# Optimization experiments

Measured on AMD Instinct MI355X. Metric: run time of the kernel, lower is better.

## Reference

```python
import jax, jax.numpy as jnp
import numpy as np

W = 131072          # window size (number of observed frames)
J = 21              # number of joints
B = J - 1           # number of bones
F, PX, PY = 512.0, 512.0, 288.0   # pinhole intrinsics (SIZE_X=1024, SIZE_Y=576)
EPS = 1e-8
WEIGHTS = {"proj": 0.25, "lift": 0.25, "bone": 0.25, "smooth": 0.25}


def _euler_batch(roll, pitch, yaw):
    """Vectorized ZYX euler -> rotation matrices, numpy, [N,3,3]."""
    cr, sr = np.cos(roll), np.sin(roll)
    cp, sp = np.cos(pitch), np.sin(pitch)
    cy, sy = np.cos(yaw), np.sin(yaw)
    R = np.empty(roll.shape + (3, 3), np.float32)
    R[..., 0, 0] = cy * cp; R[..., 0, 1] = cy * sp * sr - sy * cr; R[..., 0, 2] = cy * sp * cr + sy * sr
    R[..., 1, 0] = sy * cp; R[..., 1, 1] = sy * sp * sr + cy * cr; R[..., 1, 2] = sy * sp * cr - cy * sr
    R[..., 2, 0] = -sp;     R[..., 2, 1] = cp * sr;                R[..., 2, 2] = cp * cr
    return R


def setup_inputs() -> dict:
    key = jax.random.key(0)
    ks = jax.random.split(key, 7)
    pose3d = jax.random.normal(ks[0], (W + 1, 3, J), jnp.float32)
    bone_2d = jax.random.normal(ks[1], (W, 2, J), jnp.float32)
    lift_dirs = jax.random.normal(ks[2], (W, 3, B), jnp.float32)
    # small proper drone rotations so the projection depth stays well away from 0
    ang = 0.05 * np.asarray(jax.random.normal(ks[3], (W, 3)))
    R_drone = jnp.asarray(_euler_batch(ang[:, 0], ang[:, 1], ang[:, 2]))
    # drone positions offset so pose - C_drone ~ +10 in every coordinate
    C_drone = 0.1 * jax.random.normal(ks[4], (W, 3, 1), jnp.float32) - 10.0
    bone_lengths = jax.random.uniform(ks[5], (B,), jnp.float32, 0.5, 1.5)
    R_cam = jnp.asarray(_euler_batch(np.zeros(1), np.full(1, np.pi / 2), np.zeros(1))[0])
    # chain skeleton: bone i connects joint i+1 -> joint i
    bone_connections = jnp.stack([jnp.arange(1, J, dtype=jnp.int32),
                                  jnp.arange(0, J - 1, dtype=jnp.int32)], axis=1)
    return {"pose3d": pose3d, "bone_2d": bone_2d, "lift_dirs": lift_dirs,
            "R_drone": R_drone, "C_drone": C_drone, "bone_lengths": bone_lengths,
            "R_cam": R_cam, "bone_connections": bone_connections}


def _forward(pose3d, bone_2d, lift_dirs, R_drone, C_drone, bone_lengths, R_cam,
             bone_connections):
    Jn = pose3d.shape[2]
    b0 = bone_connections[:, 0]
    b1 = bone_connections[:, 1]
    p = pose3d[1:]                                   # [W,3,J] frames with observations

    # ---- projection loss: cam = R_cam @ R_drone^T @ (p - C_drone), pinhole
    rel = p - C_drone                                # [W,3,J]
    cam = jnp.einsum('ij,wkj,wkn->win', R_cam, R_drone, rel)  # [W,3,J]
    z = cam[:, 2]
    proj2d = jnp.stack([F * cam[:, 0] / z + PX,
                        F * cam[:, 1] / z + PY], axis=1)       # [W,2,J]
    proj_loss = jnp.sum((proj2d - bone_2d) ** 2) / (2 * Jn)

    # ---- lift loss: unit bone direction vectors vs lifted directions
    bv = p[:, :, b0] - p[:, :, b1]                   # [W,3,B]
    dirs = bv / (jnp.linalg.norm(bv, axis=1, keepdims=True) + EPS)
    lift_loss = jnp.sum((lift_dirs - dirs) ** 2) / (3 * Jn)

    # ---- bone-length loss over all W+1 frames (squared lengths, as in torch code)
    bvall = pose3d[:, :, b0] - pose3d[:, :, b1]      # [W+1,3,B]
    blen = jnp.sum(bvall ** 2, axis=1)               # [W+1,B]
    bone_loss = jnp.sum((bone_lengths[None, :] - blen) ** 2) / (Jn - 1)

    # ---- smoothness: second difference of the pose trajectory
    d = pose3d[1:] - pose3d[:-1]                     # [W,3,J]
    smooth_loss = jnp.sum((d[1:] - d[:-1]) ** 2) / (3 * Jn)

    return (WEIGHTS["proj"] * proj_loss + WEIGHTS["lift"] * lift_loss
            + WEIGHTS["bone"] * bone_loss + WEIGHTS["smooth"] * smooth_loss)


def reference(pose3d, bone_2d, lift_dirs, R_drone, C_drone, bone_lengths, R_cam,
              bone_connections):
    return _forward(pose3d, bone_2d, lift_dirs, R_drone, C_drone, bone_lengths,
                    R_cam, bone_connections)
```

## Files before the change

### kernel.cpp

```cpp
#include <hip/hip_runtime.h>

namespace {

constexpr int JN = 21;
constexpr int BN = 20;
constexpr int FR = 64;
constexpr int HT = 32;
constexpr int SPLIT0 = 36;

constexpr float F_F  = 512.0f;
constexpr float PX_F = 512.0f;
constexpr float PY_F = 288.0f;
constexpr float EPS_F = 1e-8f;

constexpr float WPROJ   = 0.25f / (2.0f * 21.0f);
constexpr float WLIFT   = 0.25f / (3.0f * 21.0f);
constexpr float WBONE   = 0.25f / 20.0f;
constexpr float WSMOOTH = 0.25f / (3.0f * 21.0f);

__device__ __forceinline__ double block_reduce(double val) {
    __shared__ double smem[16];
    const int lane = threadIdx.x & 63;
    const int wid  = threadIdx.x >> 6;
    #pragma unroll
    for (int off = 32; off > 0; off >>= 1)
        val += __shfl_down(val, off, 64);
    if (lane == 0) smem[wid] = val;
    __syncthreads();
    if (wid == 0) {
        const int nw = blockDim.x >> 6;
        val = (lane < nw) ? smem[lane] : 0.0;
        #pragma unroll
        for (int off = 32; off > 0; off >>= 1)
            val += __shfl_down(val, off, 64);
    }
    return val;
}

__global__ __launch_bounds__(256) void pose_loss_kernel(
    const float* __restrict__ pose3d,
    const float* __restrict__ bone_2d,
    const float* __restrict__ lift_dirs,
    const float* __restrict__ R_drone,
    const float* __restrict__ C_drone,
    const float* __restrict__ bone_len,
    const float* __restrict__ R_cam,
    float* __restrict__ partials,
    int W)
{
    __shared__ alignas(16) float s_pose[(FR + 2) * 63 + 2];
    __shared__ alignas(16) float s_M[FR * 12];

    const int tid = threadIdx.x;
    const int w0  = blockIdx.x * FR;
    const int nF  = min(FR, W - w0);
    const int nPoseF = min(FR + 2, W + 1 - w0);

    auto stage4 = [&](float* dst, const float* src, int nfl) {
        const int n4 = nfl >> 2;
        const float4* s4 = (const float4*)src;
        float4* d4 = (float4*)dst;
        for (int i = tid; i < n4; i += 256) d4[i] = s4[i];
        for (int i = (n4 << 2) + tid; i < nfl; i += 256) dst[i] = src[i];
    };

    auto computeM = [&](int base) {
        const int f = base + tid;
        if (tid < HT && f < nF) {
            const float* Rd = R_drone + (size_t)(w0 + f) * 9;
            float rd[9];
            #pragma unroll
            for (int k = 0; k < 9; ++k) rd[k] = Rd[k];
            float rc[9];
            #pragma unroll
            for (int k = 0; k < 9; ++k) rc[k] = R_cam[k];
            float M[9];
            #pragma unroll
            for (int i = 0; i < 3; ++i)
                #pragma unroll
                for (int k = 0; k < 3; ++k)
                    M[i * 3 + k] = rc[i * 3 + 0] * rd[k * 3 + 0]
                                 + rc[i * 3 + 1] * rd[k * 3 + 1]
                                 + rc[i * 3 + 2] * rd[k * 3 + 2];
            const float* Cp = C_drone + (size_t)(w0 + f) * 3;
            const float C0 = Cp[0], C1 = Cp[1], C2 = Cp[2];
            #pragma unroll
            for (int k = 0; k < 9; ++k) s_M[f * 12 + k] = M[k];
            #pragma unroll
            for (int i = 0; i < 3; ++i)
                s_M[f * 12 + 9 + i] =
                    M[i * 3 + 0] * C0 + M[i * 3 + 1] * C1 + M[i * 3 + 2] * C2;
        }
    };

    float partial = 0.0f;

    auto item = [&](int wl, int j) {
        const int w = w0 + wl;

        const float* P1 = s_pose + (wl + 1) * 63;
        const float p1x = P1[j];
        const float p1y = P1[JN + j];
        const float p1z = P1[2 * JN + j];

        {
            const float4 m0 = *(const float4*)(s_M + wl * 12);
            const float4 m1 = *(const float4*)(s_M + wl * 12 + 4);
            const float4 m2 = *(const float4*)(s_M + wl * 12 + 8);
            const float c0 = m0.x * p1x + m0.y * p1y + m0.z * p1z - m2.y;
            const float c1 = m0.w * p1x + m1.x * p1y + m1.y * p1z - m2.z;
            const float c2 = m1.z * p1x + m1.w * p1y + m2.x * p1z - m2.w;
            const float invz = 1.0f / c2;
            const float u = F_F * c0 * invz + PX_F;
            const float v = F_F * c1 * invz + PY_F;
            const float du = u - bone_2d[(size_t)w * 42 + j];
            const float dv = v - bone_2d[(size_t)w * 42 + JN + j];
            partial += WPROJ * (du * du + dv * dv);
        }

        if (j < BN) {
            const int b0 = j + 1;
            const int b1 = j;
            {
                const float ax = P1[b0]          - P1[b1];
                const float ay = P1[JN + b0]     - P1[JN + b1];
                const float az = P1[2 * JN + b0] - P1[2 * JN + b1];
                const float inv = 1.0f / (sqrtf(ax * ax + ay * ay + az * az) + EPS_F);
                const float lx = lift_dirs[(size_t)w * 60 + j]          - ax * inv;
                const float ly = lift_dirs[(size_t)w * 60 + BN + j]     - ay * inv;
                const float lz = lift_dirs[(size_t)w * 60 + 2 * BN + j] - az * inv;
                partial += WLIFT * (lx * lx + ly * ly + lz * lz);
            }
            const float blj = bone_len[j];
            {
                const float* P0 = s_pose + wl * 63;
                const float bx = P0[b0]          - P0[b1];
                const float by = P0[JN + b0]     - P0[JN + b1];
                const float bz = P0[2 * JN + b0] - P0[2 * JN + b1];
                const float bl = bx * bx + by * by + bz * bz;
                const float e = blj - bl;
                partial += WBONE * (e * e);
            }
            if (w == W - 1) {
                const float bx = P1[b0]          - P1[b1];
                const float by = P1[JN + b0]     - P1[JN + b1];
                const float bz = P1[2 * JN + b0] - P1[2 * JN + b1];
                const float bl = bx * bx + by * by + bz * bz;
                const float e = blj - bl;
                partial += WBONE * (e * e);
            }
        }

        if (w < W - 1) {
            const float* P0 = s_pose + wl * 63;
            const float* P2 = s_pose + (wl + 2) * 63;
            const float sx = P2[j]          - 2.0f * p1x + P0[j];
            const float sy = P2[JN + j]     - 2.0f * p1y + P0[JN + j];
            const float sz = P2[2 * JN + j] - 2.0f * p1z + P0[2 * JN + j];
            partial += WSMOOTH * (sx * sx + sy * sy + sz * sz);
        }
    };

    {
        const int f1 = min(SPLIT0, nPoseF);
        stage4(s_pose, pose3d + (size_t)w0 * 63, f1 * 63);
        computeM(0);
    }
    __syncthreads();

    if (nPoseF > SPLIT0) {
        stage4(s_pose + SPLIT0 * 63, pose3d + ((size_t)w0 + SPLIT0) * 63,
               (nPoseF - SPLIT0) * 63);
    }
    computeM(HT);

    {
        const int nItems0 = min(HT, nF) * JN;
        for (int it = tid; it < nItems0; it += 256) {
            const int wl = it / JN;
            const int j  = it - wl * JN;
            item(wl, j);
        }
    }
    __syncthreads();

    if (nF > HT) {
        const int nItems1 = (nF - HT) * JN;
        for (int it = tid; it < nItems1; it += 256) {
            const int wl = HT + it / JN;
            const int j  = it - (it / JN) * JN;
            item(wl, j);
        }
    }

    const double bsum = block_reduce((double)partial);
    if (tid == 0) partials[blockIdx.x] = (float)bsum;
}

__global__ __launch_bounds__(256) void final_reduce_kernel(
    const float* __restrict__ partials, float* __restrict__ out, int n)
{
    double v = 0.0;
    for (int i = threadIdx.x; i < n; i += blockDim.x)
        v += (double)partials[i];
    v = block_reduce(v);
    if (threadIdx.x == 0) out[0] = (float)v;
}

}

extern "C" void kernel_launch(void* const* d_in, const int* in_sizes, int n_in,
                              void* d_out, int out_size, void* d_ws, size_t ws_size,
                              hipStream_t stream) {
    const float* pose3d    = (const float*)d_in[0];
    const float* bone_2d   = (const float*)d_in[1];
    const float* lift_dirs = (const float*)d_in[2];
    const float* R_drone   = (const float*)d_in[3];
    const float* C_drone   = (const float*)d_in[4];
    const float* bone_len  = (const float*)d_in[5];
    const float* R_cam     = (const float*)d_in[6];
    float* out = (float*)d_out;
    float* partials = (float*)d_ws;

    const int W = in_sizes[3] / 9;
    const int grid = (W + FR - 1) / FR;

    pose_loss_kernel<<<grid, 256, 0, stream>>>(
        pose3d, bone_2d, lift_dirs, R_drone, C_drone, bone_len, R_cam, partials, W);
    final_reduce_kernel<<<1, 256, 0, stream>>>(partials, out, grid);
}
```

Measured before the change: 27.27 us.

## Split block work into independent per-wavefront frame slices without block barriers

Each 64-lane wavefront now stages its own 16-frame pose slice (plus 2 halo frames) and its own camera matrices into a private shared-memory region, then computes its 21x16 items. This removes the two block-wide __syncthreads and the two-phase split pipeline. It relies on wavefront-level ordering of shared-memory writes and reads. The halo frames add some redundant pose loads per wave, and the full-slice case uses a fixed unrolled item loop.

```diff
diff --git a/kernel.cpp b/kernel.cpp
--- a/kernel.cpp
+++ b/kernel.cpp
@@ -4,9 +4,10 @@
 
 constexpr int JN = 21;
 constexpr int BN = 20;
+constexpr int FW = 16;
 constexpr int FR = 64;
-constexpr int HT = 32;
-constexpr int SPLIT0 = 36;
+constexpr int SLICE = FW + 2;
+constexpr int SLICE_STRIDE = 1136;
 
 constexpr float F_F  = 512.0f;
 constexpr float PX_F = 512.0f;
@@ -48,26 +49,35 @@
     float* __restrict__ partials,
     int W)
 {
-    __shared__ alignas(16) float s_pose[(FR + 2) * 63 + 2];
-    __shared__ alignas(16) float s_M[FR * 12];
-
-    const int tid = threadIdx.x;
+    __shared__ alignas(16) float s_pose[4][SLICE_STRIDE];
+    __shared__ alignas(16) float s_M[4][FW * 12];
+
+    const int tid  = threadIdx.x;
+    const int lane = tid & 63;
+    const int wid  = tid >> 6;
+
     const int w0  = blockIdx.x * FR;
-    const int nF  = min(FR, W - w0);
-    const int nPoseF = min(FR + 2, W + 1 - w0);
-
-    auto stage4 = [&](float* dst, const float* src, int nfl) {
-        const int n4 = nfl >> 2;
-        const float4* s4 = (const float4*)src;
-        float4* d4 = (float4*)dst;
-        for (int i = tid; i < n4; i += 256) d4[i] = s4[i];
-        for (int i = (n4 << 2) + tid; i < nfl; i += 256) dst[i] = src[i];
-    };
-
-    auto computeM = [&](int base) {
-        const int f = base + tid;
-        if (tid < HT && f < nF) {
-            const float* Rd = R_drone + (size_t)(w0 + f) * 9;
+    const int fw0 = w0 + wid * FW;
+    const int nFw = min(FW, W - fw0);
+    float* myPose = s_pose[wid];
+    float* myM    = s_M[wid];
+
+    float partial = 0.0f;
+
+    if (nFw > 0) {
+        {
+            const int nSliceF = min(SLICE, W + 1 - fw0);
+            const int nfl = nSliceF * 63;
+            const float* src = pose3d + (size_t)fw0 * 63;
+            const int n4 = nfl >> 2;
+            const float4* s4 = (const float4*)src;
+            float4* d4 = (float4*)myPose;
+            for (int i = lane; i < n4; i += 64) d4[i] = s4[i];
+            for (int i = (n4 << 2) + lane; i < nfl; i += 64) myPose[i] = src[i];
+        }
+
+        if (lane < FW && lane < nFw) {
+            const float* Rd = R_drone + (size_t)(fw0 + lane) * 9;
             float rd[9];
             #pragma unroll
             for (int k = 0; k < 9; ++k) rd[k] = Rd[k];
@@ -82,114 +92,95 @@
                     M[i * 3 + k] = rc[i * 3 + 0] * rd[k * 3 + 0]
                                  + rc[i * 3 + 1] * rd[k * 3 + 1]
                                  + rc[i * 3 + 2] * rd[k * 3 + 2];
-            const float* Cp = C_drone + (size_t)(w0 + f) * 3;
+            const float* Cp = C_drone + (size_t)(fw0 + lane) * 3;
             const float C0 = Cp[0], C1 = Cp[1], C2 = Cp[2];
             #pragma unroll
-            for (int k = 0; k < 9; ++k) s_M[f * 12 + k] = M[k];
+            for (int k = 0; k < 9; ++k) myM[lane * 12 + k] = M[k];
             #pragma unroll
             for (int i = 0; i < 3; ++i)
-                s_M[f * 12 + 9 + i] =
+                myM[lane * 12 + 9 + i] =
                     M[i * 3 + 0] * C0 + M[i * 3 + 1] * C1 + M[i * 3 + 2] * C2;
         }
-    };
-
-    float partial = 0.0f;
-
-    auto item = [&](int wl, int j) {
-        const int w = w0 + wl;
-
-        const float* P1 = s_pose + (wl + 1) * 63;
-        const float p1x = P1[j];
-        const float p1y = P1[JN + j];
-        const float p1z = P1[2 * JN + j];
-
-        {
-            const float4 m0 = *(const float4*)(s_M + wl * 12);
-            const float4 m1 = *(const float4*)(s_M + wl * 12 + 4);
-            const float4 m2 = *(const float4*)(s_M + wl * 12 + 8);
-            const float c0 = m0.x * p1x + m0.y * p1y + m0.z * p1z - m2.y;
-            const float c1 = m0.w * p1x + m1.x * p1y + m1.y * p1z - m2.z;
-            const float c2 = m1.z * p1x + m1.w * p1y + m2.x * p1z - m2.w;
-            const float invz = 1.0f / c2;
-            const float u = F_F * c0 * invz + PX_F;
-            const float v = F_F * c1 * invz + PY_F;
-            const float du = u - bone_2d[(size_t)w * 42 + j];
-            const float dv = v - bone_2d[(size_t)w * 42 + JN + j];
-            partial += WPROJ * (du * du + dv * dv);
-        }
-
-        if (j < BN) {
-            const int b0 = j + 1;
-            const int b1 = j;
+
+        auto item = [&](int wl, int j) {
+            const int w = fw0 + wl;
+
+            const float* P1 = myPose + (wl + 1) * 63;
+            const float p1x = P1[j];
+            const float p1y = P1[JN + j];
+            const float p1z = P1[2 * JN + j];
+
             {
-                const float ax = P1[b0]          - P1[b1];
-                const float ay = P1[JN + b0]     - P1[JN + b1];
-                const float az = P1[2 * JN + b0] - P1[2 * JN + b1];
-                const float inv = 1.0f / (sqrtf(ax * ax + ay * ay + az * az) + EPS_F);
-                const float lx = lift_dirs[(size_t)w * 60 + j]          - ax * inv;
-                const float ly = lift_dirs[(size_t)w * 60 + BN + j]     - ay * inv;
-                const float lz = lift_dirs[(size_t)w * 60 + 2 * BN + j] - az * inv;
-                partial += WLIFT * (lx * lx + ly * ly + lz * lz);
-            }
-            const float blj = bone_len[j];
-            {
-                const float* P0 = s_pose + wl * 63;
-                const float bx = P0[b0]          - P0[b1];
-                const float by = P0[JN + b0]     - P0[JN + b1];
-                const float bz = P0[2 * JN + b0] - P0[2 * JN + b1];
-                const float bl = bx * bx + by * by + bz * bz;
-                const float e = blj - bl;
-                partial += WBONE * (e * e);
-            }
-            if (w == W - 1) {
-                const float bx = P1[b0]          - P1[b1];
-                const float by = P1[JN + b0]     - P1[JN + b1];
-                const float bz = P1[2 * JN + b0] - P1[2 * JN + b1];
-                const float bl = bx * bx + by * by + bz * bz;
-                const float e = blj - bl;
-                partial += WBONE * (e * e);
-            }
-        }
-
-        if (w < W - 1) {
-            const float* P0 = s_pose + wl * 63;
-            const float* P2 = s_pose + (wl + 2) * 63;
-            const float sx = P2[j]          - 2.0f * p1x + P0[j];
-            const float sy = P2[JN + j]     - 2.0f * p1y + P0[JN + j];
-            const float sz = P2[2 * JN + j] - 2.0f * p1z + P0[2 * JN + j];
-            partial += WSMOOTH * (sx * sx + sy * sy + sz * sz);
-        }
-    };
-
-    {
-        const int f1 = min(SPLIT0, nPoseF);
-        stage4(s_pose, pose3d + (size_t)w0 * 63, f1 * 63);
-        computeM(0);
-    }
-    __syncthreads();
-
-    if (nPoseF > SPLIT0) {
-        stage4(s_pose + SPLIT0 * 63, pose3d + ((size_t)w0 + SPLIT0) * 63,
-               (nPoseF - SPLIT0) * 63);
-    }
-    computeM(HT);
-
-    {
-        const int nItems0 = min(HT, nF) * JN;
-        for (int it = tid; it < nItems0; it += 256) {
-            const int wl = it / JN;
-            const int j  = it - wl * JN;
-            item(wl, j);
-        }
-    }
-    __syncthreads();
-
-    if (nF > HT) {
-        const int nItems1 = (nF - HT) * JN;
-        for (int it = tid; it < nItems1; it += 256) {
-            const int wl = HT + it / JN;
-            const int j  = it - (it / JN) * JN;
-            item(wl, j);
+                const float4 m0 = *(const float4*)(myM + wl * 12);
+                const float4 m1 = *(const float4*)(myM + wl * 12 + 4);
+                const float4 m2 = *(const float4*)(myM + wl * 12 + 8);
+                const float c0 = m0.x * p1x + m0.y * p1y + m0.z * p1z - m2.y;
+                const float c1 = m0.w * p1x + m1.x * p1y + m1.y * p1z - m2.z;
+                const float c2 = m1.z * p1x + m1.w * p1y + m2.x * p1z - m2.w;
+                const float invz = 1.0f / c2;
+                const float u = F_F * c0 * invz + PX_F;
+                const float v = F_F * c1 * invz + PY_F;
+                const float du = u - bone_2d[(size_t)w * 42 + j];
+                const float dv = v - bone_2d[(size_t)w * 42 + JN + j];
+                partial += WPROJ * (du * du + dv * dv);
+            }
+
+            if (j < BN) {
+                const int b0 = j + 1;
+                const int b1 = j;
+                {
+                    const float ax = P1[b0]          - P1[b1];
+                    const float ay = P1[JN + b0]     - P1[JN + b1];
+                    const float az = P1[2 * JN + b0] - P1[2 * JN + b1];
+                    const float inv = 1.0f / (sqrtf(ax * ax + ay * ay + az * az) + EPS_F);
+                    const float lx = lift_dirs[(size_t)w * 60 + j]          - ax * inv;
+                    const float ly = lift_dirs[(size_t)w * 60 + BN + j]     - ay * inv;
+                    const float lz = lift_dirs[(size_t)w * 60 + 2 * BN + j] - az * inv;
+                    partial += WLIFT * (lx * lx + ly * ly + lz * lz);
+                }
+                const float blj = bone_len[j];
+                {
+                    const float* P0 = myPose + wl * 63;
+                    const float bx = P0[b0]          - P0[b1];
+                    const float by = P0[JN + b0]     - P0[JN + b1];
+                    const float bz = P0[2 * JN + b0] - P0[2 * JN + b1];
+                    const float bl = bx * bx + by * by + bz * bz;
+                    const float e = blj - bl;
+                    partial += WBONE * (e * e);
+                }
+                if (w == W - 1) {
+                    const float bx = P1[b0]          - P1[b1];
+                    const float by = P1[JN + b0]     - P1[JN + b1];
+                    const float bz = P1[2 * JN + b0] - P1[2 * JN + b1];
+                    const float bl = bx * bx + by * by + bz * bz;
+                    const float e = blj - bl;
+                    partial += WBONE * (e * e);
+                }
+            }
+
+            if (w < W - 1) {
+                const float* P0 = myPose + wl * 63;
+                const float* P2 = myPose + (wl + 2) * 63;
+                const float sx = P2[j]          - 2.0f * p1x + P0[j];
+                const float sy = P2[JN + j]     - 2.0f * p1y + P0[JN + j];
+                const float sz = P2[2 * JN + j] - 2.0f * p1z + P0[2 * JN + j];
+                partial += WSMOOTH * (sx * sx + sy * sy + sz * sz);
+            }
+        };
+
+        if (nFw == FW) {
+            #pragma unroll
+            for (int k = 0; k < 5; ++k) {
+                const int it = k * 64 + lane;
+                item(it / JN, it - (it / JN) * JN);
+            }
+            if (lane < 16) {
+                const int it = 5 * 64 + lane;
+                item(it / JN, it - (it / JN) * JN);
+            }
+        } else {
+            for (int it = lane; it < nFw * JN; it += 64)
+                item(it / JN, it - (it / JN) * JN);
         }
     }
 
```

Measured after the change: 28.91 us. 1.06x slower.

## Process four joints per thread with vectorized loads and single-stage staging

Applied to the files above, without the earlier changes.

Replaces the per-(frame,joint) work item with chunks of four joints per thread, so neighbouring pose values are loaded once into registers and reused across the projection, lift, bone and smoothness terms. lift_dirs and bone_len are now read as float4. The two-phase staged pipeline (split pose copy and split M computation with overlapped work) becomes one full stage followed by a single barrier. This cuts the shared-memory reads and divisions per element, but 384 chunks over 256 threads leaves the second pass half-occupied and removes the previous load/compute overlap.

```diff
diff --git a/kernel.cpp b/kernel.cpp
--- a/kernel.cpp
+++ b/kernel.cpp
@@ -5,8 +5,6 @@
 constexpr int JN = 21;
 constexpr int BN = 20;
 constexpr int FR = 64;
-constexpr int HT = 32;
-constexpr int SPLIT0 = 36;
 
 constexpr float F_F  = 512.0f;
 constexpr float PX_F = 512.0f;
@@ -56,141 +54,166 @@
     const int nF  = min(FR, W - w0);
     const int nPoseF = min(FR + 2, W + 1 - w0);
 
-    auto stage4 = [&](float* dst, const float* src, int nfl) {
+    {
+        const float* src = pose3d + (size_t)w0 * 63;
+        const int nfl = nPoseF * 63;
         const int n4 = nfl >> 2;
         const float4* s4 = (const float4*)src;
-        float4* d4 = (float4*)dst;
+        float4* d4 = (float4*)s_pose;
         for (int i = tid; i < n4; i += 256) d4[i] = s4[i];
-        for (int i = (n4 << 2) + tid; i < nfl; i += 256) dst[i] = src[i];
+        for (int i = (n4 << 2) + tid; i < nfl; i += 256) s_pose[i] = src[i];
+    }
+
+    if (tid < FR && tid < nF) {
+        const float* Rd = R_drone + (size_t)(w0 + tid) * 9;
+        float rd[9];
+        #pragma unroll
+        for (int k = 0; k < 9; ++k) rd[k] = Rd[k];
+        float rc[9];
+        #pragma unroll
+        for (int k = 0; k < 9; ++k) rc[k] = R_cam[k];
+        float M[9];
+        #pragma unroll
+        for (int i = 0; i < 3; ++i)
+            #pragma unroll
+            for (int k = 0; k < 3; ++k)
+                M[i * 3 + k] = rc[i * 3 + 0] * rd[k * 3 + 0]
+                             + rc[i * 3 + 1] * rd[k * 3 + 1]
+                             + rc[i * 3 + 2] * rd[k * 3 + 2];
+        const float* Cp = C_drone + (size_t)(w0 + tid) * 3;
+        const float C0 = Cp[0], C1 = Cp[1], C2 = Cp[2];
+        #pragma unroll
+        for (int k = 0; k < 9; ++k) s_M[tid * 12 + k] = M[k];
+        #pragma unroll
+        for (int i = 0; i < 3; ++i)
+            s_M[tid * 12 + 9 + i] =
+                M[i * 3 + 0] * C0 + M[i * 3 + 1] * C1 + M[i * 3 + 2] * C2;
+    }
+    __syncthreads();
+
+    float partial = 0.0f;
+
+    auto chunkFull = [&](int wl, int k) {
+        const int w  = w0 + wl;
+        const int j0 = 4 * k;
+        const float* P1 = s_pose + (wl + 1) * 63 + j0;
+        const float* P0 = s_pose + wl * 63 + j0;
+
+        float p1x[5], p1y[5], p1z[5], p0x[5], p0y[5], p0z[5];
+        #pragma unroll
+        for (int t = 0; t < 5; ++t) {
+            p1x[t] = P1[t]; p1y[t] = P1[21 + t]; p1z[t] = P1[42 + t];
+            p0x[t] = P0[t]; p0y[t] = P0[21 + t]; p0z[t] = P0[42 + t];
+        }
+
+        const float4 m0 = *(const float4*)(s_M + wl * 12);
+        const float4 m1 = *(const float4*)(s_M + wl * 12 + 4);
+        const float4 m2 = *(const float4*)(s_M + wl * 12 + 8);
+
+        #pragma unroll
+        for (int t = 0; t < 4; ++t) {
+            const float c0 = m0.x * p1x[t] + m0.y * p1y[t] + m0.z * p1z[t] - m2.y;
+            const float c1 = m0.w * p1x[t] + m1.x * p1y[t] + m1.y * p1z[t] - m2.z;
+            const float c2 = m1.z * p1x[t] + m1.w * p1y[t] + m2.x * p1z[t] - m2.w;
+            const float invz = 1.0f / c2;
+            const float du = F_F * c0 * invz + PX_F - bone_2d[(size_t)w * 42 + j0 + t];
+            const float dv = F_F * c1 * invz + PY_F - bone_2d[(size_t)w * 42 + 21 + j0 + t];
+            partial += WPROJ * (du * du + dv * dv);
+        }
+
+        {
+            const float4 lx = *(const float4*)(lift_dirs + (size_t)w * 60 + j0);
+            const float4 ly = *(const float4*)(lift_dirs + (size_t)w * 60 + 20 + j0);
+            const float4 lz = *(const float4*)(lift_dirs + (size_t)w * 60 + 40 + j0);
+            const float lxa[4] = {lx.x, lx.y, lx.z, lx.w};
+            const float lya[4] = {ly.x, ly.y, ly.z, ly.w};
+            const float lza[4] = {lz.x, lz.y, lz.z, lz.w};
+            #pragma unroll
+            for (int t = 0; t < 4; ++t) {
+                const float ax = p1x[t + 1] - p1x[t];
+                const float ay = p1y[t + 1] - p1y[t];
+                const float az = p1z[t + 1] - p1z[t];
+                const float inv = 1.0f / (sqrtf(ax * ax + ay * ay + az * az) + EPS_F);
+                const float dx = lxa[t] - ax * inv;
+                const float dy = lya[t] - ay * inv;
+                const float dz = lza[t] - az * inv;
+                partial += WLIFT * (dx * dx + dy * dy + dz * dz);
+            }
+        }
+
+        {
+            const float4 bl = *(const float4*)(bone_len + j0);
+            const float bla[4] = {bl.x, bl.y, bl.z, bl.w};
+            #pragma unroll
+            for (int t = 0; t < 4; ++t) {
+                const float bx = p0x[t + 1] - p0x[t];
+                const float by = p0y[t + 1] - p0y[t];
+                const float bz = p0z[t + 1] - p0z[t];
+                const float e = bla[t] - (bx * bx + by * by + bz * bz);
+                partial += WBONE * (e * e);
+            }
+            if (w == W - 1) {
+                #pragma unroll
+                for (int t = 0; t < 4; ++t) {
+                    const float bx = p1x[t + 1] - p1x[t];
+                    const float by = p1y[t + 1] - p1y[t];
+                    const float bz = p1z[t + 1] - p1z[t];
+                    const float e = bla[t] - (bx * bx + by * by + bz * bz);
+                    partial += WBONE * (e * e);
+                }
+            }
+        }
+
+        if (w < W - 1) {
+            const float* P2 = P0 + 126;
+            #pragma unroll
+            for (int t = 0; t < 4; ++t) {
+                const float sx = P2[t]      - 2.0f * p1x[t] + p0x[t];
+                const float sy = P2[21 + t] - 2.0f * p1y[t] + p0y[t];
+                const float sz = P2[42 + t] - 2.0f * p1z[t] + p0z[t];
+                partial += WSMOOTH * (sx * sx + sy * sy + sz * sz);
+            }
+        }
     };
 
-    auto computeM = [&](int base) {
-        const int f = base + tid;
-        if (tid < HT && f < nF) {
-            const float* Rd = R_drone + (size_t)(w0 + f) * 9;
-            float rd[9];
-            #pragma unroll
-            for (int k = 0; k < 9; ++k) rd[k] = Rd[k];
-            float rc[9];
-            #pragma unroll
-            for (int k = 0; k < 9; ++k) rc[k] = R_cam[k];
-            float M[9];
-            #pragma unroll
-            for (int i = 0; i < 3; ++i)
-                #pragma unroll
-                for (int k = 0; k < 3; ++k)
-                    M[i * 3 + k] = rc[i * 3 + 0] * rd[k * 3 + 0]
-                                 + rc[i * 3 + 1] * rd[k * 3 + 1]
-                                 + rc[i * 3 + 2] * rd[k * 3 + 2];
-            const float* Cp = C_drone + (size_t)(w0 + f) * 3;
-            const float C0 = Cp[0], C1 = Cp[1], C2 = Cp[2];
-            #pragma unroll
-            for (int k = 0; k < 9; ++k) s_M[f * 12 + k] = M[k];
-            #pragma unroll
-            for (int i = 0; i < 3; ++i)
-                s_M[f * 12 + 9 + i] =
-                    M[i * 3 + 0] * C0 + M[i * 3 + 1] * C1 + M[i * 3 + 2] * C2;
+    auto chunkLast = [&](int wl) {
+        const int w = w0 + wl;
+        const float* P1 = s_pose + (wl + 1) * 63 + 20;
+        const float* P0 = s_pose + wl * 63 + 20;
+        const float p1x = P1[0], p1y = P1[21], p1z = P1[42];
+
+        const float4 m0 = *(const float4*)(s_M + wl * 12);
+        const float4 m1 = *(const float4*)(s_M + wl * 12 + 4);
+        const float4 m2 = *(const float4*)(s_M + wl * 12 + 8);
+        const float c0 = m0.x * p1x + m0.y * p1y + m0.z * p1z - m2.y;
+        const float c1 = m0.w * p1x + m1.x * p1y + m1.y * p1z - m2.z;
+        const float c2 = m1.z * p1x + m1.w * p1y + m2.x * p1z - m2.w;
+        const float invz = 1.0f / c2;
+        const float du = F_F * c0 * invz + PX_F - bone_2d[(size_t)w * 42 + 20];
+        const float dv = F_F * c1 * invz + PY_F - bone_2d[(size_t)w * 42 + 41];
+        partial += WPROJ * (du * du + dv * dv);
+
+        if (w < W - 1) {
+            const float* P2 = P0 + 126;
+            const float sx = P2[0]  - 2.0f * p1x + P0[0];
+            const float sy = P2[21] - 2.0f * p1y + P0[21];
+            const float sz = P2[42] - 2.0f * p1z + P0[42];
+            partial += WSMOOTH * (sx * sx + sy * sy + sz * sz);
         }
     };
 
-    float partial = 0.0f;
-
-    auto item = [&](int wl, int j) {
-        const int w = w0 + wl;
-
-        const float* P1 = s_pose + (wl + 1) * 63;
-        const float p1x = P1[j];
-        const float p1y = P1[JN + j];
-        const float p1z = P1[2 * JN + j];
-
-        {
-            const float4 m0 = *(const float4*)(s_M + wl * 12);
-            const float4 m1 = *(const float4*)(s_M + wl * 12 + 4);
-            const float4 m2 = *(const float4*)(s_M + wl * 12 + 8);
-            const float c0 = m0.x * p1x + m0.y * p1y + m0.z * p1z - m2.y;
-            const float c1 = m0.w * p1x + m1.x * p1y + m1.y * p1z - m2.z;
-            const float c2 = m1.z * p1x + m1.w * p1y + m2.x * p1z - m2.w;
-            const float invz = 1.0f / c2;
-            const float u = F_F * c0 * invz + PX_F;
-            const float v = F_F * c1 * invz + PY_F;
-            const float du = u - bone_2d[(size_t)w * 42 + j];
-            const float dv = v - bone_2d[(size_t)w * 42 + JN + j];
-            partial += WPROJ * (du * du + dv * dv);
-        }
-
-        if (j < BN) {
-            const int b0 = j + 1;
-            const int b1 = j;
-            {
-                const float ax = P1[b0]          - P1[b1];
-                const float ay = P1[JN + b0]     - P1[JN + b1];
-                const float az = P1[2 * JN + b0] - P1[2 * JN + b1];
-                const float inv = 1.0f / (sqrtf(ax * ax + ay * ay + az * az) + EPS_F);
-                const float lx = lift_dirs[(size_t)w * 60 + j]          - ax * inv;
-                const float ly = lift_dirs[(size_t)w * 60 + BN + j]     - ay * inv;
-                const float lz = lift_dirs[(size_t)w * 60 + 2 * BN + j] - az * inv;
-                partial += WLIFT * (lx * lx + ly * ly + lz * lz);
-            }
-            const float blj = bone_len[j];
-            {
-                const float* P0 = s_pose + wl * 63;
-                const float bx = P0[b0]          - P0[b1];
-                const float by = P0[JN + b0]     - P0[JN + b1];
-                const float bz = P0[2 * JN + b0] - P0[2 * JN + b1];
-                const float bl = bx * bx + by * by + bz * bz;
-                const float e = blj - bl;
-                partial += WBONE * (e * e);
-            }
-            if (w == W - 1) {
-                const float bx = P1[b0]          - P1[b1];
-                const float by = P1[JN + b0]     - P1[JN + b1];
-                const float bz = P1[2 * JN + b0] - P1[2 * JN + b1];
-                const float bl = bx * bx + by * by + bz * bz;
-                const float e = blj - bl;
-                partial += WBONE * (e * e);
-            }
-        }
-
-        if (w < W - 1) {
-            const float* P0 = s_pose + wl * 63;
-            const float* P2 = s_pose + (wl + 2) * 63;
-            const float sx = P2[j]          - 2.0f * p1x + P0[j];
-            const float sy = P2[JN + j]     - 2.0f * p1y + P0[JN + j];
-            const float sz = P2[2 * JN + j] - 2.0f * p1z + P0[2 * JN + j];
-            partial += WSMOOTH * (sx * sx + sy * sy + sz * sz);
-        }
+    auto doChunk = [&](int cid) {
+        const int wl = cid / 6;
+        const int k  = cid - wl * 6;
+        if (k < 5) chunkFull(wl, k);
+        else       chunkLast(wl);
     };
 
-    {
-        const int f1 = min(SPLIT0, nPoseF);
-        stage4(s_pose, pose3d + (size_t)w0 * 63, f1 * 63);
-        computeM(0);
-    }
-    __syncthreads();
-
-    if (nPoseF > SPLIT0) {
-        stage4(s_pose + SPLIT0 * 63, pose3d + ((size_t)w0 + SPLIT0) * 63,
-               (nPoseF - SPLIT0) * 63);
-    }
-    computeM(HT);
-
-    {
-        const int nItems0 = min(HT, nF) * JN;
-        for (int it = tid; it < nItems0; it += 256) {
-            const int wl = it / JN;
-            const int j  = it - wl * JN;
-            item(wl, j);
-        }
-    }
-    __syncthreads();
-
-    if (nF > HT) {
-        const int nItems1 = (nF - HT) * JN;
-        for (int it = tid; it < nItems1; it += 256) {
-            const int wl = HT + it / JN;
-            const int j  = it - (it / JN) * JN;
-            item(wl, j);
-        }
+    if (nF == FR) {
+        doChunk(tid);
+        if (tid < FR * 6 - 256) doChunk(256 + tid);
+    } else {
+        for (int c = tid; c < nF * 6; c += 256) doChunk(c);
     }
 
     const double bsum = block_reduce((double)partial);
```

New measurement: 28.28 us. 1.04x slower.
